# Optimization experiments

Hardware: AMD Instinct MI355X
Metric: run time of the kernel (lower is better)

The kernel has to match this reference:

```python
import jax, jax.numpy as jnp
import numpy as np

N_NODES = 100_000
E_OFF = 1_500_000
LATENT = 64
MP_STEPS = 3


def setup_inputs() -> dict:
    key = jax.random.key(0)
    ks = jax.random.split(key, 12)
    # lower-triangular graph: all self-loops + random off-diagonal edges with row >= col
    r = jax.random.randint(ks[0], (E_OFF,), 0, N_NODES)
    c = jax.random.randint(ks[1], (E_OFF,), 0, N_NODES)
    diag = jnp.arange(N_NODES)
    edge_row = jnp.concatenate([jnp.maximum(r, c), diag]).astype(jnp.int64)
    edge_col = jnp.concatenate([jnp.minimum(r, c), diag]).astype(jnp.int64)
    E = E_OFF + N_NODES
    # positive weights (gcn_norm takes deg^{-1/2} of weighted degree)
    edge_attr = jax.random.uniform(ks[2], (E,), jnp.float32) + 0.05
    x = jax.random.normal(ks[3], (N_NODES, 1), jnp.float32)
    L = LATENT
    def lin(k, fi, fo):
        return jax.random.normal(k, (fi, fo), jnp.float32) / np.sqrt(fi)
    return {
        "x": x,
        "edge_attr": edge_attr,
        "w_enc": lin(ks[4], 1, L), "b_enc": jnp.zeros((L,), jnp.float32),
        "conv1_w": jax.random.normal(ks[5], (MP_STEPS, L, L), jnp.float32) / np.sqrt(L),
        "conv1_b": jnp.zeros((MP_STEPS, L), jnp.float32),
        "conv2_w": jax.random.normal(ks[6], (MP_STEPS, L, L), jnp.float32) / np.sqrt(L),
        "conv2_b": jnp.zeros((MP_STEPS, L), jnp.float32),
        "dec_w1": lin(ks[7], 2 * L, L), "dec_b1": jnp.zeros((L,), jnp.float32),
        "dec_w2": lin(ks[8], L, 1), "dec_b2": jnp.zeros((1,), jnp.float32),
        "edge_row": edge_row,
        "edge_col": edge_col,
    }


def reference(x, edge_attr, w_enc, b_enc, conv1_w, conv1_b, conv2_w, conv2_b,
              dec_w1, dec_b1, dec_w2, dec_b2, edge_row, edge_col):
    N = x.shape[0]
    # GCN normalization (graph already contains all self-loops, so PyG's
    # add_remaining_self_loops is a no-op and keeps existing loop weights)
    deg = jax.ops.segment_sum(edge_attr, edge_col, num_segments=N)
    dinv = jnp.where(deg > 0, jax.lax.rsqrt(jnp.maximum(deg, 1e-30)), 0.0)
    norm = dinv[edge_row] * edge_attr * dinv[edge_col]  # [E]
    cnt = jnp.maximum(
        jax.ops.segment_sum(jnp.ones_like(edge_attr), edge_col, num_segments=N), 1.0
    )[:, None]  # mean aggregation denominator

    def gcn(h, W, b):
        m = (h @ W)[edge_row] * norm[:, None]           # [E, F] messages
        agg = jax.ops.segment_sum(m, edge_col, num_segments=N) / cnt
        return agg + b

    # node encoder: single Linear (no activation)
    h = x @ w_enc + b_enc
    for i in range(MP_STEPS):
        h = jax.nn.relu(gcn(h, conv1_w[i], conv1_b[i]))
        h = jax.nn.relu(gcn(h, conv2_w[i], conv2_b[i]))

    # edge decoder: gather endpoints, MLP [2L -> L -> 1]
    e = jnp.concatenate([h[edge_row], h[edge_col]], axis=1)
    e = jax.nn.relu(e @ dec_w1 + dec_b1)
    e = (e @ dec_w2 + dec_b2)[:, 0]                      # [E]
    vals = jnp.where(edge_row == edge_col, jax.nn.softplus(e), e)
    return vals
```

## Files before the change

### kernel.cpp

```cpp
#include <hip/hip_runtime.h>
#include <hip/hip_fp16.h>
#include <math.h>

#define L 64
#define FIXS 65536.0f
#define WAITCNT_LGKM0 0xC07F

static __device__ __forceinline__ __half2 h2add(__half2 a, __half2 b) {
    return __half2{__hadd(a.x, b.x), __hadd(a.y, b.y)};
}
static __device__ __forceinline__ __half2 h2relu(__half2 a) {
    const __half z = __float2half(0.f);
    return __half2{__hgt(a.x, z) ? a.x : z, __hgt(a.y, z) ? a.y : z};
}


__global__ void k_hist(const int* __restrict__ col, const float* __restrict__ attr,
                       unsigned* __restrict__ degcnt,
                       int* __restrict__ rank, int E) {
    int e = blockIdx.x * blockDim.x + threadIdx.x;
    if (e < E) {
        int c = col[e];
        unsigned fx = (unsigned)(int)rintf(attr[e] * FIXS);
        unsigned old = atomicAdd(&degcnt[c], (1u << 24) | fx);
        rank[e] = (int)(old >> 24);
    }
}

__global__ void k_dinv(const unsigned* __restrict__ degcnt,
                       float* __restrict__ dinv, int* __restrict__ cntI,
                       float* __restrict__ rcnt, int N) {
    int n = blockIdx.x * blockDim.x + threadIdx.x;
    if (n < N) {
        unsigned p = degcnt[n];
        unsigned cnt = p >> 24;
        float d = (float)(p & 0xFFFFFFu) * (1.0f / FIXS);
        dinv[n] = (d > 0.f) ? (1.0f / sqrtf(fmaxf(d, 1e-30f))) : 0.f;
        cntI[n] = (int)cnt;
        unsigned c = cnt ? cnt : 1u;
        rcnt[n] = 1.0f / (float)c;
    }
}


__global__ __launch_bounds__(256) void k_scan_a(const int* __restrict__ cntI,
                                                int* __restrict__ blockSums, int N) {
    __shared__ int red[4];
    int b = blockIdx.x, t = threadIdx.x;
    int base = b * 1024 + t * 4;
    int s = 0;
    #pragma unroll
    for (int i = 0; i < 4; ++i) { int idx = base + i; if (idx < N) s += cntI[idx]; }
    #pragma unroll
    for (int off = 32; off > 0; off >>= 1) s += __shfl_down(s, off);
    if ((t & 63) == 0) red[t >> 6] = s;
    __syncthreads();
    if (t == 0) blockSums[b] = red[0] + red[1] + red[2] + red[3];
}

__global__ __launch_bounds__(1024) void k_scan_b(int* __restrict__ blockSums, int B,
                                                 int* __restrict__ ptr, int N) {
    __shared__ int sh[1024];
    int t = threadIdx.x;
    sh[t] = (t < B) ? blockSums[t] : 0;
    __syncthreads();
    for (int off = 1; off < 1024; off <<= 1) {
        int v = (t >= off) ? sh[t - off] : 0;
        __syncthreads();
        sh[t] += v;
        __syncthreads();
    }
    if (t < B) blockSums[t] = (t == 0) ? 0 : sh[t - 1];
    if (t == B - 1) ptr[N] = sh[t];
}

__global__ __launch_bounds__(256) void k_scan_c(const int* __restrict__ cntI,
                                                const int* __restrict__ blockSums,
                                                int* __restrict__ ptr, int N) {
    __shared__ int th[256];
    int b = blockIdx.x, t = threadIdx.x;
    int base = b * 1024 + t * 4;
    int v[4]; int s = 0;
    #pragma unroll
    for (int i = 0; i < 4; ++i) {
        int idx = base + i;
        v[i] = (idx < N) ? cntI[idx] : 0;
        s += v[i];
    }
    th[t] = s;
    __syncthreads();
    for (int off = 1; off < 256; off <<= 1) {
        int x = (t >= off) ? th[t - off] : 0;
        __syncthreads();
        th[t] += x;
        __syncthreads();
    }
    int pre = ((t == 0) ? 0 : th[t - 1]) + blockSums[b];
    #pragma unroll
    for (int i = 0; i < 4; ++i) {
        int idx = base + i;
        if (idx < N) ptr[idx] = pre;
        pre += v[i];
    }
}

__global__ void k_scatter(const int* __restrict__ row, const int* __restrict__ col,
                          const float* __restrict__ attr, const float* __restrict__ dinv,
                          const int* __restrict__ colptr,
                          int* __restrict__ rank ,
                          unsigned* __restrict__ csrX, int E) {
    int e = blockIdx.x * blockDim.x + threadIdx.x;
    if (e < E) {
        int r = row[e], c = col[e];
        int pos = colptr[c] + rank[e];
        float nrm = dinv[r] * attr[e] * dinv[c];
        unsigned short nb = __half_as_ushort(__float2half(nrm));
        csrX[pos] = (unsigned)r | ((unsigned)nb << 17);
        rank[e] = pos;
    }
}


__global__ void k_encode(const float* __restrict__ x, const float* __restrict__ w_enc,
                         const float* __restrict__ b_enc, __half* __restrict__ h, int N) {
    int idx = blockIdx.x * blockDim.x + threadIdx.x;
    if (idx < N * L) {
        int n = idx >> 6, f = idx & 63;
        h[idx] = __float2half(x[n] * w_enc[f] + b_enc[f]);
    }
}


__global__ __launch_bounds__(256) void k_gcn(const uint2* __restrict__ h_in2,
        __half* __restrict__ h_out,
        const float* __restrict__ W, const float* __restrict__ bias,
        const int* __restrict__ colptr, const unsigned* __restrict__ csrX,
        const float* __restrict__ rcnt, int N) {
    __shared__ float sm[4][72];
    int lane = threadIdx.x & 63;
    int warp = threadIdx.x >> 6;
    int grp  = lane >> 4;
    int sub  = lane & 15;
    int wid  = (blockIdx.x * blockDim.x + threadIdx.x) >> 6;
    int nw   = (gridDim.x * blockDim.x) >> 6;
    float* smw = &sm[warp][0];

    float Wc[L];
    #pragma unroll
    for (int f = 0; f < L; ++f) Wc[f] = W[f * L + lane];
    float bl = bias[lane];

    for (int n = wid; n < N; n += nw) {
        int beg = colptr[n], end = colptr[n + 1];
        float4 sA = make_float4(0.f, 0.f, 0.f, 0.f);
        float4 sB = make_float4(0.f, 0.f, 0.f, 0.f);
        float4 sC = make_float4(0.f, 0.f, 0.f, 0.f);
        float4 sD = make_float4(0.f, 0.f, 0.f, 0.f);
        for (int base = beg; base < end; base += 64) {
            int m = end - base; if (m > 64) m = 64;
            unsigned mw = 0;
            if (lane < m) mw = csrX[base + lane];
            int kmax = (m + 3) >> 2;
            int k = 0;
            for (; k + 4 <= kmax; k += 4) {
                int j0 = 4 * k + grp;
                unsigned x0 = (unsigned)__shfl((int)mw, j0);
                unsigned x1 = (unsigned)__shfl((int)mw, j0 + 4);
                unsigned x2 = (unsigned)__shfl((int)mw, j0 + 8);
                unsigned x3 = (unsigned)__shfl((int)mw, j0 + 12);
                int r0 = (int)(x0 & 0x1FFFFu), r1 = (int)(x1 & 0x1FFFFu);
                int r2 = (int)(x2 & 0x1FFFFu), r3 = (int)(x3 & 0x1FFFFu);
                float w0 = __half2float(__ushort_as_half((unsigned short)(x0 >> 17)));
                float w1 = __half2float(__ushort_as_half((unsigned short)(x1 >> 17)));
                float w2 = __half2float(__ushort_as_half((unsigned short)(x2 >> 17)));
                float w3 = __half2float(__ushort_as_half((unsigned short)(x3 >> 17)));
                uint2 q0 = h_in2[(size_t)r0 * 16 + sub];
                uint2 q1 = h_in2[(size_t)r1 * 16 + sub];
                uint2 q2 = h_in2[(size_t)r2 * 16 + sub];
                uint2 q3 = h_in2[(size_t)r3 * 16 + sub];
                float2 l0 = __half22float2(*(__half2*)&q0.x), g0 = __half22float2(*(__half2*)&q0.y);
                float2 l1 = __half22float2(*(__half2*)&q1.x), g1 = __half22float2(*(__half2*)&q1.y);
                float2 l2 = __half22float2(*(__half2*)&q2.x), g2 = __half22float2(*(__half2*)&q2.y);
                float2 l3 = __half22float2(*(__half2*)&q3.x), g3 = __half22float2(*(__half2*)&q3.y);
                sA.x += w0 * l0.x; sA.y += w0 * l0.y; sA.z += w0 * g0.x; sA.w += w0 * g0.y;
                sB.x += w1 * l1.x; sB.y += w1 * l1.y; sB.z += w1 * g1.x; sB.w += w1 * g1.y;
                sC.x += w2 * l2.x; sC.y += w2 * l2.y; sC.z += w2 * g2.x; sC.w += w2 * g2.y;
                sD.x += w3 * l3.x; sD.y += w3 * l3.y; sD.z += w3 * g3.x; sD.w += w3 * g3.y;
            }
            for (; k < kmax; ++k) {
                int j0 = 4 * k + grp;
                unsigned x0 = (unsigned)__shfl((int)mw, j0);
                int   r0 = (int)(x0 & 0x1FFFFu);
                float w0 = __half2float(__ushort_as_half((unsigned short)(x0 >> 17)));
                uint2 q0 = h_in2[(size_t)r0 * 16 + sub];
                float2 l0 = __half22float2(*(__half2*)&q0.x), g0 = __half22float2(*(__half2*)&q0.y);
                sA.x += w0 * l0.x; sA.y += w0 * l0.y; sA.z += w0 * g0.x; sA.w += w0 * g0.y;
            }
        }
        float4 s;
        s.x = (sA.x + sB.x) + (sC.x + sD.x);
        s.y = (sA.y + sB.y) + (sC.y + sD.y);
        s.z = (sA.z + sB.z) + (sC.z + sD.z);
        s.w = (sA.w + sB.w) + (sC.w + sD.w);
        s.x += __shfl_xor(s.x, 16); s.x += __shfl_xor(s.x, 32);
        s.y += __shfl_xor(s.y, 16); s.y += __shfl_xor(s.y, 32);
        s.z += __shfl_xor(s.z, 16); s.z += __shfl_xor(s.z, 32);
        s.w += __shfl_xor(s.w, 16); s.w += __shfl_xor(s.w, 32);
        if (grp == 0) {
            smw[4 * sub + 0] = s.x; smw[4 * sub + 1] = s.y;
            smw[4 * sub + 2] = s.z; smw[4 * sub + 3] = s.w;
        }
        __builtin_amdgcn_s_waitcnt(WAITCNT_LGKM0);
        float a0 = 0.f, a1 = 0.f, a2 = 0.f, a3 = 0.f;
        const float4* smv = (const float4*)smw;
        #pragma unroll
        for (int q = 0; q < 16; ++q) {
            float4 sv = smv[q];
            a0 += sv.x * Wc[4 * q + 0];
            a1 += sv.y * Wc[4 * q + 1];
            a2 += sv.z * Wc[4 * q + 2];
            a3 += sv.w * Wc[4 * q + 3];
        }
        float o = ((a0 + a1) + (a2 + a3)) * rcnt[n] + bl;
        h_out[(size_t)n * L + lane] = __float2half(fmaxf(o, 0.f));
    }
}


__global__ __launch_bounds__(256) void k_mv2(const __half* __restrict__ h,
        const float* __restrict__ W1, const float* __restrict__ b1,
        __half* __restrict__ U, __half* __restrict__ V, int N) {
    __shared__ float sm[4][72];
    int lane = threadIdx.x & 63;
    int warp = threadIdx.x >> 6;
    int wid  = (blockIdx.x * blockDim.x + threadIdx.x) >> 6;
    int nw   = (gridDim.x * blockDim.x) >> 6;
    float* smw = &sm[warp][0];
    float Wu[L], Wv[L];
    #pragma unroll
    for (int f = 0; f < L; ++f) Wu[f] = W1[f * L + lane];
    #pragma unroll
    for (int f = 0; f < L; ++f) Wv[f] = W1[(L + f) * L + lane];
    float bl = b1[lane];
    for (int n = wid; n < N; n += nw) {
        float hl = __half2float(h[(size_t)n * L + lane]);
        smw[lane] = hl;
        __builtin_amdgcn_s_waitcnt(WAITCNT_LGKM0);
        float a0 = 0.f, a1 = 0.f, c0 = 0.f, c1 = 0.f;
        const float4* smv = (const float4*)smw;
        #pragma unroll
        for (int q = 0; q < 16; ++q) {
            float4 sv = smv[q];
            a0 += sv.x * Wu[4 * q + 0] ; a1 += sv.y * Wu[4 * q + 1];
            a0 += sv.z * Wu[4 * q + 2] ; a1 += sv.w * Wu[4 * q + 3];
            c0 += sv.x * Wv[4 * q + 0] ; c1 += sv.y * Wv[4 * q + 1];
            c0 += sv.z * Wv[4 * q + 2] ; c1 += sv.w * Wv[4 * q + 3];
        }
        U[(size_t)n * L + lane] = __float2half((a0 + a1) + bl);
        V[(size_t)n * L + lane] = __float2half(c0 + c1);
        __builtin_amdgcn_s_waitcnt(WAITCNT_LGKM0);
    }
}


__global__ __launch_bounds__(256) void k_edge(const __half* __restrict__ U,
        const __half* __restrict__ V, const float* __restrict__ w2,
        const float* __restrict__ b2,
        const int* __restrict__ colptr, const unsigned* __restrict__ csrX,
        float* __restrict__ tmp, int N) {
    int lane = threadIdx.x & 63;
    int half = lane & 1;
    int wid  = (blockIdx.x * blockDim.x + threadIdx.x) >> 6;
    int nw   = (gridDim.x * blockDim.x) >> 6;
    float w2f[32];
    #pragma unroll
    for (int k = 0; k < 32; ++k) w2f[k] = w2[32 * half + k];
    float b2v = b2[0];

    for (int n = wid; n < N; n += nw) {
        int beg = colptr[n], end = colptr[n + 1];
        const uint4* vrow = (const uint4*)(V + (size_t)n * L + 32 * half);
        uint4 v0 = vrow[0], v1 = vrow[1], v2 = vrow[2], v3 = vrow[3];
        for (int base = beg; base < end; base += 32) {
            int epos = base + (lane >> 1);
            if (epos < end) {
                unsigned md = csrX[epos];
                int r = (int)(md & 0x1FFFFu);
                const uint4* urow = (const uint4*)(U + (size_t)r * L + 32 * half);
                uint4 u0 = urow[0], u1 = urow[1], u2 = urow[2], u3 = urow[3];
                float p = 0.f;
                #define DOT8(uq, vq, B) { \
                    __half2 ta = h2relu(h2add(*(__half2*)&(uq).x, *(__half2*)&(vq).x)); \
                    __half2 tb = h2relu(h2add(*(__half2*)&(uq).y, *(__half2*)&(vq).y)); \
                    __half2 tc = h2relu(h2add(*(__half2*)&(uq).z, *(__half2*)&(vq).z)); \
                    __half2 td = h2relu(h2add(*(__half2*)&(uq).w, *(__half2*)&(vq).w)); \
                    float2 fa = __half22float2(ta), fb = __half22float2(tb); \
                    float2 fc = __half22float2(tc), fd = __half22float2(td); \
                    p += fa.x * w2f[B+0] + fa.y * w2f[B+1] + fb.x * w2f[B+2] + fb.y * w2f[B+3]; \
                    p += fc.x * w2f[B+4] + fc.y * w2f[B+5] + fd.x * w2f[B+6] + fd.y * w2f[B+7]; }
                DOT8(u0, v0, 0) DOT8(u1, v1, 8) DOT8(u2, v2, 16) DOT8(u3, v3, 24)
                #undef DOT8
                p += __shfl_xor(p, 1);
                if (half == 0) {
                    float val = p + b2v;
                    if (r == n) val = fmaxf(val, 0.f) + log1pf(expf(-fabsf(val)));
                    tmp[epos] = val;
                }
            }
        }
    }
}


__global__ void k_perm(const int* __restrict__ epos, const float* __restrict__ tmp,
                       float* __restrict__ out, int E) {
    int e = blockIdx.x * blockDim.x + threadIdx.x;
    if (e < E) out[e] = tmp[epos[e]];
}


extern "C" void kernel_launch(void* const* d_in, const int* in_sizes, int n_in,
                              void* d_out, int out_size, void* d_ws, size_t ws_size,
                              hipStream_t stream) {
    const float* x     = (const float*)d_in[0];
    const float* attr  = (const float*)d_in[1];
    const float* w_enc = (const float*)d_in[2];
    const float* b_enc = (const float*)d_in[3];
    const float* c1w   = (const float*)d_in[4];
    const float* c1b   = (const float*)d_in[5];
    const float* c2w   = (const float*)d_in[6];
    const float* c2b   = (const float*)d_in[7];
    const float* dw1   = (const float*)d_in[8];
    const float* db1   = (const float*)d_in[9];
    const float* dw2   = (const float*)d_in[10];
    const float* db2   = (const float*)d_in[11];
    const int*   erow  = (const int*)d_in[12];
    const int*   ecol  = (const int*)d_in[13];
    int N = in_sizes[0];
    int E = in_sizes[1];
    float* out = (float*)d_out;

    char* w = (char*)d_ws;
    auto alloc = [&](size_t bytes) {
        char* p = w; w += (bytes + 255) & ~(size_t)255; return p;
    };
    unsigned* degcnt = (unsigned*)alloc((size_t)N * 4);
    size_t zbytes = (size_t)(w - (char*)d_ws);
    float* dinv   = (float*)alloc((size_t)N * 4);
    int*   cntI   = (int*)  alloc((size_t)N * 4);
    float* rcnt   = (float*)alloc((size_t)N * 4);
    int*   colptr = (int*)  alloc((size_t)(N + 1) * 4);
    int*   bsums  = (int*)  alloc(((size_t)(N + 1023) / 1024 + 1) * 4);
    int*   rank   = (int*)  alloc((size_t)E * 4);
    unsigned* csrX = (unsigned*)alloc((size_t)E * 4);
    float* tmp    = (float*)alloc((size_t)E * 4);
    __half* hA    = (__half*)alloc((size_t)N * L * 2);
    __half* hB    = (__half*)alloc((size_t)N * L * 2);
    __half* hU    = (__half*)alloc((size_t)N * L * 2);
    __half* hV    = (__half*)alloc((size_t)N * L * 2);
    (void)ws_size; (void)n_in; (void)out_size;

    (void)hipMemsetAsync(d_ws, 0, zbytes, stream);

    int eb = (E + 255) / 256;
    int nb = (N + 255) / 256;
    int B  = (N + 1023) / 1024;
    k_hist<<<eb, 256, 0, stream>>>(ecol, attr, degcnt, rank, E);
    k_dinv<<<nb, 256, 0, stream>>>(degcnt, dinv, cntI, rcnt, N);
    k_scan_a<<<B, 256, 0, stream>>>(cntI, bsums, N);
    k_scan_b<<<1, 1024, 0, stream>>>(bsums, B, colptr, N);
    k_scan_c<<<B, 256, 0, stream>>>(cntI, bsums, colptr, N);
    k_scatter<<<eb, 256, 0, stream>>>(erow, ecol, attr, dinv, colptr, rank, csrX, E);
    k_encode<<<(N * L + 255) / 256, 256, 0, stream>>>(x, w_enc, b_enc, hA, N);

    __half* hin = hA; __half* hout = hB;
    for (int i = 0; i < 3; ++i) {
        k_gcn<<<2048, 256, 0, stream>>>((const uint2*)hin, hout, c1w + i * L * L,
                                        c1b + i * L, colptr, csrX, rcnt, N);
        __half* t = hin; hin = hout; hout = t;
        k_gcn<<<2048, 256, 0, stream>>>((const uint2*)hin, hout, c2w + i * L * L,
                                        c2b + i * L, colptr, csrX, rcnt, N);
        t = hin; hin = hout; hout = t;
    }
    k_mv2<<<2048, 256, 0, stream>>>(hin, dw1, db1, hU, hV, N);
    k_edge<<<2048, 256, 0, stream>>>(hU, hV, dw2, db2, colptr, csrX, tmp, N);
    k_perm<<<eb, 256, 0, stream>>>(rank, tmp, out, E);
}
```

Measured before the change: 680.1 us.

## Prefetch next node's CSR metadata and use fma_mix / packed-f16 inline asm

In both the GCN aggregation kernel and the edge decoder, each warp now loads the next node's column range and its first chunk of packed edge words before it finishes the current node. This overlaps that dependent-load latency with compute. The fp16-to-fp32 convert-and-FMA sequences are replaced with v_fma_mix_f32 inline asm, and the decoder's add+relu uses v_pk_add_f16/v_pk_max_f16. The asm and the extra live registers may hurt scheduling or occupancy.

```diff
diff --git a/kernel.cpp b/kernel.cpp
--- a/kernel.cpp
+++ b/kernel.cpp
@@ -6,13 +6,15 @@
 #define FIXS 65536.0f
 #define WAITCNT_LGKM0 0xC07F
 
-static __device__ __forceinline__ __half2 h2add(__half2 a, __half2 b) {
-    return __half2{__hadd(a.x, b.x), __hadd(a.y, b.y)};
-}
-static __device__ __forceinline__ __half2 h2relu(__half2 a) {
-    const __half z = __float2half(0.f);
-    return __half2{__hgt(a.x, z) ? a.x : z, __hgt(a.y, z) ? a.y : z};
-}
+#define FMAMIX_LO(acc, pkh, ws) \
+    asm("v_fma_mix_f32 %0, %1, %2, %0 op_sel:[0,0,0] op_sel_hi:[1,0,0]" \
+        : "+v"(acc) : "v"(pkh), "v"(ws))
+#define FMAMIX_HI(acc, pkh, ws) \
+    asm("v_fma_mix_f32 %0, %1, %2, %0 op_sel:[1,0,0] op_sel_hi:[1,0,0]" \
+        : "+v"(acc) : "v"(pkh), "v"(ws))
+#define PKADDRELU(d, a, b) \
+    asm("v_pk_add_f16 %0, %1, %2\n\tv_pk_max_f16 %0, %0, 0" \
+        : "=v"(d) : "v"(a), "v"(b))
 
 
 __global__ void k_hist(const int* __restrict__ col, const float* __restrict__ attr,
@@ -150,24 +152,30 @@
     for (int f = 0; f < L; ++f) Wc[f] = W[f * L + lane];
     float bl = bias[lane];
 
+    int beg = 0, end = 0; unsigned mw = 0;
+    if (wid < N) {
+        beg = colptr[wid];
+        end = colptr[wid + 1];
+        if (beg + lane < end) mw = csrX[beg + lane];
+    }
+
     for (int n = wid; n < N; n += nw) {
-        int beg = colptr[n], end = colptr[n + 1];
-        float4 sA = make_float4(0.f, 0.f, 0.f, 0.f);
-        float4 sB = make_float4(0.f, 0.f, 0.f, 0.f);
-        float4 sC = make_float4(0.f, 0.f, 0.f, 0.f);
-        float4 sD = make_float4(0.f, 0.f, 0.f, 0.f);
-        for (int base = beg; base < end; base += 64) {
-            int m = end - base; if (m > 64) m = 64;
-            unsigned mw = 0;
-            if (lane < m) mw = csrX[base + lane];
-            int kmax = (m + 3) >> 2;
+        int n2 = n + nw;
+        int beg2 = 0, end2 = 0;
+        if (n2 < N) { beg2 = colptr[n2]; end2 = colptr[n2 + 1]; }
+
+        float sA0=0.f,sA1=0.f,sA2=0.f,sA3=0.f, sB0=0.f,sB1=0.f,sB2=0.f,sB3=0.f;
+        float sC0=0.f,sC1=0.f,sC2=0.f,sC3=0.f, sD0=0.f,sD1=0.f,sD2=0.f,sD3=0.f;
+
+        auto PROC = [&](unsigned mwv, int mm) {
+            int kmax = (mm + 3) >> 2;
             int k = 0;
             for (; k + 4 <= kmax; k += 4) {
                 int j0 = 4 * k + grp;
-                unsigned x0 = (unsigned)__shfl((int)mw, j0);
-                unsigned x1 = (unsigned)__shfl((int)mw, j0 + 4);
-                unsigned x2 = (unsigned)__shfl((int)mw, j0 + 8);
-                unsigned x3 = (unsigned)__shfl((int)mw, j0 + 12);
+                unsigned x0 = (unsigned)__shfl((int)mwv, j0);
+                unsigned x1 = (unsigned)__shfl((int)mwv, j0 + 4);
+                unsigned x2 = (unsigned)__shfl((int)mwv, j0 + 8);
+                unsigned x3 = (unsigned)__shfl((int)mwv, j0 + 12);
                 int r0 = (int)(x0 & 0x1FFFFu), r1 = (int)(x1 & 0x1FFFFu);
                 int r2 = (int)(x2 & 0x1FFFFu), r3 = (int)(x3 & 0x1FFFFu);
                 float w0 = __half2float(__ushort_as_half((unsigned short)(x0 >> 17)));
@@ -178,37 +186,49 @@
                 uint2 q1 = h_in2[(size_t)r1 * 16 + sub];
                 uint2 q2 = h_in2[(size_t)r2 * 16 + sub];
                 uint2 q3 = h_in2[(size_t)r3 * 16 + sub];
-                float2 l0 = __half22float2(*(__half2*)&q0.x), g0 = __half22float2(*(__half2*)&q0.y);
-                float2 l1 = __half22float2(*(__half2*)&q1.x), g1 = __half22float2(*(__half2*)&q1.y);
-                float2 l2 = __half22float2(*(__half2*)&q2.x), g2 = __half22float2(*(__half2*)&q2.y);
-                float2 l3 = __half22float2(*(__half2*)&q3.x), g3 = __half22float2(*(__half2*)&q3.y);
-                sA.x += w0 * l0.x; sA.y += w0 * l0.y; sA.z += w0 * g0.x; sA.w += w0 * g0.y;
-                sB.x += w1 * l1.x; sB.y += w1 * l1.y; sB.z += w1 * g1.x; sB.w += w1 * g1.y;
-                sC.x += w2 * l2.x; sC.y += w2 * l2.y; sC.z += w2 * g2.x; sC.w += w2 * g2.y;
-                sD.x += w3 * l3.x; sD.y += w3 * l3.y; sD.z += w3 * g3.x; sD.w += w3 * g3.y;
+                FMAMIX_LO(sA0, q0.x, w0); FMAMIX_HI(sA1, q0.x, w0);
+                FMAMIX_LO(sA2, q0.y, w0); FMAMIX_HI(sA3, q0.y, w0);
+                FMAMIX_LO(sB0, q1.x, w1); FMAMIX_HI(sB1, q1.x, w1);
+                FMAMIX_LO(sB2, q1.y, w1); FMAMIX_HI(sB3, q1.y, w1);
+                FMAMIX_LO(sC0, q2.x, w2); FMAMIX_HI(sC1, q2.x, w2);
+                FMAMIX_LO(sC2, q2.y, w2); FMAMIX_HI(sC3, q2.y, w2);
+                FMAMIX_LO(sD0, q3.x, w3); FMAMIX_HI(sD1, q3.x, w3);
+                FMAMIX_LO(sD2, q3.y, w3); FMAMIX_HI(sD3, q3.y, w3);
             }
             for (; k < kmax; ++k) {
                 int j0 = 4 * k + grp;
-                unsigned x0 = (unsigned)__shfl((int)mw, j0);
+                unsigned x0 = (unsigned)__shfl((int)mwv, j0);
                 int   r0 = (int)(x0 & 0x1FFFFu);
                 float w0 = __half2float(__ushort_as_half((unsigned short)(x0 >> 17)));
                 uint2 q0 = h_in2[(size_t)r0 * 16 + sub];
-                float2 l0 = __half22float2(*(__half2*)&q0.x), g0 = __half22float2(*(__half2*)&q0.y);
-                sA.x += w0 * l0.x; sA.y += w0 * l0.y; sA.z += w0 * g0.x; sA.w += w0 * g0.y;
+                FMAMIX_LO(sA0, q0.x, w0); FMAMIX_HI(sA1, q0.x, w0);
+                FMAMIX_LO(sA2, q0.y, w0); FMAMIX_HI(sA3, q0.y, w0);
             }
-        }
-        float4 s;
-        s.x = (sA.x + sB.x) + (sC.x + sD.x);
-        s.y = (sA.y + sB.y) + (sC.y + sD.y);
-        s.z = (sA.z + sB.z) + (sC.z + sD.z);
-        s.w = (sA.w + sB.w) + (sC.w + sD.w);
-        s.x += __shfl_xor(s.x, 16); s.x += __shfl_xor(s.x, 32);
-        s.y += __shfl_xor(s.y, 16); s.y += __shfl_xor(s.y, 32);
-        s.z += __shfl_xor(s.z, 16); s.z += __shfl_xor(s.z, 32);
-        s.w += __shfl_xor(s.w, 16); s.w += __shfl_xor(s.w, 32);
+        };
+
+        int m = end - beg; if (m > 64) m = 64;
+        PROC(mw, m);
+        for (int base = beg + 64; base < end; base += 64) {
+            int mm = end - base; if (mm > 64) mm = 64;
+            unsigned mwc = 0;
+            if (lane < mm) mwc = csrX[base + lane];
+            PROC(mwc, mm);
+        }
+
+        unsigned mw2 = 0;
+        if (n2 < N && beg2 + lane < end2) mw2 = csrX[beg2 + lane];
+
+        float sx = (sA0 + sB0) + (sC0 + sD0);
+        float sy = (sA1 + sB1) + (sC1 + sD1);
+        float sz = (sA2 + sB2) + (sC2 + sD2);
+        float sw = (sA3 + sB3) + (sC3 + sD3);
+        sx += __shfl_xor(sx, 16); sx += __shfl_xor(sx, 32);
+        sy += __shfl_xor(sy, 16); sy += __shfl_xor(sy, 32);
+        sz += __shfl_xor(sz, 16); sz += __shfl_xor(sz, 32);
+        sw += __shfl_xor(sw, 16); sw += __shfl_xor(sw, 32);
         if (grp == 0) {
-            smw[4 * sub + 0] = s.x; smw[4 * sub + 1] = s.y;
-            smw[4 * sub + 2] = s.z; smw[4 * sub + 3] = s.w;
+            smw[4 * sub + 0] = sx; smw[4 * sub + 1] = sy;
+            smw[4 * sub + 2] = sz; smw[4 * sub + 3] = sw;
         }
         __builtin_amdgcn_s_waitcnt(WAITCNT_LGKM0);
         float a0 = 0.f, a1 = 0.f, a2 = 0.f, a3 = 0.f;
@@ -223,6 +243,8 @@
         }
         float o = ((a0 + a1) + (a2 + a3)) * rcnt[n] + bl;
         h_out[(size_t)n * L + lane] = __float2half(fmaxf(o, 0.f));
+
+        beg = beg2; end = end2; mw = mw2;
     }
 }
 
@@ -269,45 +291,68 @@
         const int* __restrict__ colptr, const unsigned* __restrict__ csrX,
         float* __restrict__ tmp, int N) {
     int lane = threadIdx.x & 63;
-    int half = lane & 1;
+    int hf   = lane & 1;
     int wid  = (blockIdx.x * blockDim.x + threadIdx.x) >> 6;
     int nw   = (gridDim.x * blockDim.x) >> 6;
     float w2f[32];
     #pragma unroll
-    for (int k = 0; k < 32; ++k) w2f[k] = w2[32 * half + k];
+    for (int k = 0; k < 32; ++k) w2f[k] = w2[32 * hf + k];
     float b2v = b2[0];
 
+    int beg = 0, end = 0; unsigned md0 = 0;
+    if (wid < N) {
+        beg = colptr[wid]; end = colptr[wid + 1];
+        int ep = beg + (lane >> 1);
+        if (ep < end) md0 = csrX[ep];
+    }
+
     for (int n = wid; n < N; n += nw) {
-        int beg = colptr[n], end = colptr[n + 1];
-        const uint4* vrow = (const uint4*)(V + (size_t)n * L + 32 * half);
+        int n2 = n + nw;
+        int beg2 = 0, end2 = 0;
+        if (n2 < N) { beg2 = colptr[n2]; end2 = colptr[n2 + 1]; }
+
+        const uint4* vrow = (const uint4*)(V + (size_t)n * L + 32 * hf);
         uint4 v0 = vrow[0], v1 = vrow[1], v2 = vrow[2], v3 = vrow[3];
+        unsigned md = md0;
         for (int base = beg; base < end; base += 32) {
             int epos = base + (lane >> 1);
             if (epos < end) {
-                unsigned md = csrX[epos];
                 int r = (int)(md & 0x1FFFFu);
-                const uint4* urow = (const uint4*)(U + (size_t)r * L + 32 * half);
+                const uint4* urow = (const uint4*)(U + (size_t)r * L + 32 * hf);
                 uint4 u0 = urow[0], u1 = urow[1], u2 = urow[2], u3 = urow[3];
-                float p = 0.f;
-                #define DOT8(uq, vq, B) { \
-                    __half2 ta = h2relu(h2add(*(__half2*)&(uq).x, *(__half2*)&(vq).x)); \
-                    __half2 tb = h2relu(h2add(*(__half2*)&(uq).y, *(__half2*)&(vq).y)); \
-                    __half2 tc = h2relu(h2add(*(__half2*)&(uq).z, *(__half2*)&(vq).z)); \
-                    __half2 td = h2relu(h2add(*(__half2*)&(uq).w, *(__half2*)&(vq).w)); \
-                    float2 fa = __half22float2(ta), fb = __half22float2(tb); \
-                    float2 fc = __half22float2(tc), fd = __half22float2(td); \
-                    p += fa.x * w2f[B+0] + fa.y * w2f[B+1] + fb.x * w2f[B+2] + fb.y * w2f[B+3]; \
-                    p += fc.x * w2f[B+4] + fc.y * w2f[B+5] + fd.x * w2f[B+6] + fd.y * w2f[B+7]; }
-                DOT8(u0, v0, 0) DOT8(u1, v1, 8) DOT8(u2, v2, 16) DOT8(u3, v3, 24)
-                #undef DOT8
+                float p0 = 0.f, p1 = 0.f, p2 = 0.f, p3 = 0.f;
+                #define DOT2X(uw, vw, B, pa, pb) { unsigned t_; \
+                    PKADDRELU(t_, (uw), (vw)); \
+                    FMAMIX_LO(pa, t_, w2f[B]); FMAMIX_HI(pb, t_, w2f[(B) + 1]); }
+                DOT2X(u0.x, v0.x,  0, p0, p1) DOT2X(u0.y, v0.y,  2, p2, p3)
+                DOT2X(u0.z, v0.z,  4, p0, p1) DOT2X(u0.w, v0.w,  6, p2, p3)
+                DOT2X(u1.x, v1.x,  8, p0, p1) DOT2X(u1.y, v1.y, 10, p2, p3)
+                DOT2X(u1.z, v1.z, 12, p0, p1) DOT2X(u1.w, v1.w, 14, p2, p3)
+                DOT2X(u2.x, v2.x, 16, p0, p1) DOT2X(u2.y, v2.y, 18, p2, p3)
+                DOT2X(u2.z, v2.z, 20, p0, p1) DOT2X(u2.w, v2.w, 22, p2, p3)
+                DOT2X(u3.x, v3.x, 24, p0, p1) DOT2X(u3.y, v3.y, 26, p2, p3)
+                DOT2X(u3.z, v3.z, 28, p0, p1) DOT2X(u3.w, v3.w, 30, p2, p3)
+                #undef DOT2X
+                float p = (p0 + p2) + (p1 + p3);
                 p += __shfl_xor(p, 1);
-                if (half == 0) {
+                if (hf == 0) {
                     float val = p + b2v;
                     if (r == n) val = fmaxf(val, 0.f) + log1pf(expf(-fabsf(val)));
                     tmp[epos] = val;
                 }
             }
-        }
+            if (base + 32 < end) {
+                int ep2 = base + 32 + (lane >> 1);
+                md = (ep2 < end) ? csrX[ep2] : 0;
+            }
+        }
+
+        unsigned mdn = 0;
+        if (n2 < N) {
+            int ep = beg2 + (lane >> 1);
+            if (ep < end2) mdn = csrX[ep];
+        }
+        beg = beg2; end = end2; md0 = mdn;
     }
 }
 
```

Result: faster. 649.6 us (-4.5%).
